# Kernel tuning notes

Hardware: AMD Instinct MI355X
Metric: run time of the kernel (lower is better)

Reference implementation:

```python
import jax, jax.numpy as jnp
import numpy as np
from jax import lax

B, C, H, W = 32, 64, 128, 128   # c must equal max_in_channels (see view in forward)
OUT, K = 64, 3
HIDDEN = 128


def setup_inputs() -> dict:
    key = jax.random.key(0)
    k1, k2, k3, k4, k5 = jax.random.split(key, 5)
    x = jax.random.normal(k1, (B, C, H, W), dtype=jnp.float32)
    # torch Linear default init scale ~ 1/sqrt(fan_in); use small scale for stability
    W1 = jax.random.normal(k2, (C, HIDDEN), dtype=jnp.float32) * (1.0 / np.sqrt(C))
    b1 = jax.random.normal(k3, (HIDDEN,), dtype=jnp.float32) * 0.01
    W2 = jax.random.normal(k4, (HIDDEN, OUT * C * K * K), dtype=jnp.float32) * (1.0 / np.sqrt(HIDDEN))
    b2 = jax.random.normal(k5, (OUT * C * K * K,), dtype=jnp.float32) * 0.01
    return {"x": x, "W1": W1, "b1": b1, "W2": W2, "b2": b2}


def reference(x, W1, b1, W2, b2):
    b, c, h, w = x.shape
    # per-sample channel statistics -> weight-generator MLP
    stats = jnp.mean(x, axis=(2, 3))                       # [b, c]
    hidden = jax.nn.relu(stats @ W1 + b1)                  # [b, hidden]
    weight = (hidden @ W2 + b2).reshape(b, OUT, c, K, K)   # per-sample conv kernels
    # batched per-sample conv expressed as one grouped convolution:
    # group i convolves sample i's channels with sample i's kernels
    lhs = x.reshape(1, b * c, h, w)                        # [1, b*c, H, W]
    rhs = weight.reshape(b * OUT, c, K, K)                 # [b*OUT, c, K, K]
    pad = K // 2
    out = lax.conv_general_dilated(
        lhs, rhs,
        window_strides=(1, 1),
        padding=[(pad, pad), (pad, pad)],
        feature_group_count=b,
        dimension_numbers=("NCHW", "OIHW", "NCHW"),
    )
    return out.reshape(b, OUT, h, w)
```

## Files before the change

### kernel.cpp

```cpp
#include <hip/hip_runtime.h>

typedef unsigned short u16;
typedef unsigned int   u32;
typedef __attribute__((ext_vector_type(8))) short short8v;
typedef __attribute__((ext_vector_type(4))) float float4v;
typedef __attribute__((address_space(1))) u32 g_u32;
typedef __attribute__((address_space(3))) u32 l_u32;


__device__ __forceinline__ u16 f2bf(float f) {
  u32 u = __builtin_bit_cast(u32, f);
  return (u16)((u + 0x7fffu + ((u >> 16) & 1u)) >> 16);
}

__global__ void __launch_bounds__(256) k_transpose_stats(
    const float* __restrict__ x, float* __restrict__ statsum, u16* __restrict__ xt)
{
  __shared__ u16 tile[64 * 130];
  const int b = blockIdx.x >> 7, y = blockIdx.x & 127;
  const int tid = threadIdx.x;
  const int c = tid >> 2, part = tid & 3, xb = part * 32;
  const float* src = x + (((size_t)(b * 64 + c) * 128 + y) * 128 + xb);
  float sum = 0.f;
  #pragma unroll
  for (int i = 0; i < 32; i += 4) {
    float4 v = *(const float4*)(src + i);
    sum += (v.x + v.y) + (v.z + v.w);
    ushort2 p01; p01.x = f2bf(v.x); p01.y = f2bf(v.y);
    ushort2 p23; p23.x = f2bf(v.z); p23.y = f2bf(v.w);
    *(ushort2*)&tile[c * 130 + xb + i]     = p01;
    *(ushort2*)&tile[c * 130 + xb + i + 2] = p23;
  }
  sum += __shfl_xor(sum, 1);
  sum += __shfl_xor(sum, 2);
  if (part == 0) atomicAdd(&statsum[b * 64 + c], sum);
  __syncthreads();

  uint4* xtv = (uint4*)xt;
  const size_t rowg = ((size_t)b * 130 + (y + 1)) * 1024;
  #pragma unroll
  for (int d0 = 0; d0 < 1024; d0 += 256) {
    const int d = d0 + tid;
    const int xd = d >> 3, s = d & 7;
    const int c8 = s ^ (xd & 7);
    const u16* tp = &tile[c8 * 8 * 130 + xd];
    u16 v0 = tp[0 * 130], v1 = tp[1 * 130], v2 = tp[2 * 130], v3 = tp[3 * 130];
    u16 v4 = tp[4 * 130], v5 = tp[5 * 130], v6 = tp[6 * 130], v7 = tp[7 * 130];
    uint4 g;
    g.x = (u32)v0 | ((u32)v1 << 16);
    g.y = (u32)v2 | ((u32)v3 << 16);
    g.z = (u32)v4 | ((u32)v5 << 16);
    g.w = (u32)v6 | ((u32)v7 << 16);
    xtv[rowg + d] = g;
  }
  if (y == 0 || y == 127) {
    const size_t prow = ((size_t)b * 130 + (y == 0 ? 0 : 129)) * 1024;
    uint4 z; z.x = z.y = z.z = z.w = 0u;
    #pragma unroll
    for (int d0 = 0; d0 < 1024; d0 += 256) xtv[prow + d0 + tid] = z;
  }
}

__global__ void __launch_bounds__(128) k_hidden(
    const float* __restrict__ statsum, const float* __restrict__ W1,
    const float* __restrict__ b1, float* __restrict__ hidden)
{
  const int b = blockIdx.x, h = threadIdx.x;
  float s = b1[h];
  #pragma unroll 4
  for (int c = 0; c < 64; ++c)
    s = fmaf(statsum[b * 64 + c] * (1.f / 16384.f), W1[c * 128 + h], s);
  hidden[b * 128 + h] = fmaxf(s, 0.f);
}

__global__ void __launch_bounds__(256) k_weightgen(
    const float* __restrict__ hidden, const float* __restrict__ W2,
    const float* __restrict__ b2, u16* __restrict__ wt)
{
  const int idx = blockIdx.x * 256 + threadIdx.x;
  const int b = idx >> 12, o = (idx >> 6) & 63, c = idx & 63;
  const int j0 = (o * 64 + c) * 9;
  float acc[9];
  #pragma unroll
  for (int t = 0; t < 9; ++t) acc[t] = b2[j0 + t];
  const float* hb = hidden + b * 128;
  for (int h = 0; h < 128; ++h) {
    const float hv = hb[h];
    const float* w2p = W2 + (size_t)h * 36864 + j0;
    #pragma unroll
    for (int t = 0; t < 9; ++t) acc[t] = fmaf(hv, w2p[t], acc[t]);
  }
  const int cc = c >> 5, cr = c & 31;
  #pragma unroll
  for (int kidx = 0; kidx < 9; ++kidx) {
    const size_t widx = ((size_t)(((b * 9 + kidx) * 2 + cc) * 64 + o)) * 32 + cr;
    wt[widx] = f2bf(acc[kidx]);
  }
}

__global__ void __launch_bounds__(256) k_conv(
    const u16* __restrict__ xt, const u16* __restrict__ wt, float* __restrict__ out)
{
  __shared__ u16 xs[4 * 1024 * 8];
  const int blk = blockIdx.x;
  const int b = blk >> 6, r = blk & 63;
  const int y0 = r * 2;
  const int tid = threadIdx.x;

  {
    const size_t srcg = ((size_t)b * 130 + y0) * 1024;
    #pragma unroll
    for (int k2 = 0; k2 < 16; ++k2) {
      const int g = k2 * 256 + tid;
      const void* gsrc = (const char*)xt + (srcg + (size_t)g) * 16;
      void* ldst = (char*)xs + (size_t)g * 16;
#if defined(__has_builtin) && __has_builtin(__builtin_amdgcn_global_load_lds)
      __builtin_amdgcn_global_load_lds((const g_u32*)gsrc, (l_u32*)ldst, 16, 0, 0);
#else
      *(uint4*)ldst = *(const uint4*)gsrc;
#endif
    }
  }
  __syncthreads();

  const int lane = tid & 63, wid = tid >> 6;
  const int lo = lane & 15, q = lane >> 4;
  const int yout = y0 + (wid >> 1);
  const int colbase = (wid & 1) * 64;

  const short8v z8 = {0, 0, 0, 0, 0, 0, 0, 0};
  float4v acc[4][4];
  {
    const float4v z4 = {0.f, 0.f, 0.f, 0.f};
    #pragma unroll
    for (int mt = 0; mt < 4; ++mt)
      #pragma unroll
      for (int nt = 0; nt < 4; ++nt) acc[mt][nt] = z4;
  }

  const size_t wbase = (size_t)b * 36864 + (size_t)(lo * 32 + q * 8);
  short8v a_cur[4];
  {
    const u16* p = wt + wbase;
    #pragma unroll
    for (int mt = 0; mt < 4; ++mt) a_cur[mt] = *(const short8v*)(p + mt * 512);
  }

  #pragma unroll 1
  for (int chunk = 0; chunk < 18; ++chunk) {
    const int kidx = chunk >> 1, cc = chunk & 1;
    const int ky = kidx / 3, kx = kidx - ky * 3;

    short8v a_nxt[4];
    if (chunk < 17) {
      const u16* p = wt + wbase + (size_t)(chunk + 1) * 2048;
      #pragma unroll
      for (int mt = 0; mt < 4; ++mt) a_nxt[mt] = *(const short8v*)(p + mt * 512);
    }

    const int row_l = (wid >> 1) + ky;
    const int c8 = cc * 4 + q;
    short8v bv[4];
    #pragma unroll
    for (int nt = 0; nt < 4; ++nt) {
      const int xin = colbase + nt * 16 + lo + kx - 1;
      const bool okx = ((unsigned)xin < 128u);
      const int gpos = okx ? (row_l * 1024 + xin * 8 + (c8 ^ (xin & 7))) : 0;
      short8v v = *(const short8v*)(xs + (size_t)gpos * 8);
      bv[nt] = okx ? v : z8;
    }

    #pragma unroll
    for (int mt = 0; mt < 4; ++mt)
      #pragma unroll
      for (int nt = 0; nt < 4; ++nt)
        acc[mt][nt] = __builtin_amdgcn_mfma_f32_16x16x32_bf16(
            a_cur[mt], bv[nt], acc[mt][nt], 0, 0, 0);

    if (chunk < 17) {
      #pragma unroll
      for (int mt = 0; mt < 4; ++mt) a_cur[mt] = a_nxt[mt];
    }
  }

  #pragma unroll
  for (int mt = 0; mt < 4; ++mt) {
    #pragma unroll
    for (int i = 0; i < 4; ++i) {
      const int o = mt * 16 + q * 4 + i;
      float* orow = out + ((size_t)(b * 64 + o) * 128 + yout) * 128;
      #pragma unroll
      for (int nt = 0; nt < 4; ++nt)
        orow[colbase + nt * 16 + lo] = acc[mt][nt][i];
    }
  }
}

extern "C" void kernel_launch(void* const* d_in, const int* in_sizes, int n_in,
                              void* d_out, int out_size, void* d_ws, size_t ws_size,
                              hipStream_t stream) {
  (void)in_sizes; (void)n_in; (void)out_size; (void)ws_size;
  const float* x  = (const float*)d_in[0];
  const float* W1 = (const float*)d_in[1];
  const float* b1 = (const float*)d_in[2];
  const float* W2 = (const float*)d_in[3];
  const float* b2 = (const float*)d_in[4];
  float* out = (float*)d_out;

  float* statsum = (float*)d_ws;
  float* hidden  = (float*)((char*)d_ws + 8192);
  u16*   wt      = (u16*)((char*)d_ws + 32768);
  u16*   xt      = (u16*)((char*)d_ws + (size_t)(4 << 20));

  hipMemsetAsync(statsum, 0, 2048 * sizeof(float), stream);
  k_transpose_stats<<<32 * 128, 256, 0, stream>>>(x, statsum, xt);
  k_hidden<<<32, 128, 0, stream>>>(statsum, W1, b1, hidden);
  k_weightgen<<<512, 256, 0, stream>>>(hidden, W2, b2, wt);
  k_conv<<<32 * 64, 256, 0, stream>>>(xt, wt, out);
}
```

Baseline: 353.6 us.

## Restructure weight generator so each W2 element is loaded once for all batches

The weight-generation GEMM is reorganised so each thread owns one output column j of W2 and accumulates all 32 batch samples, with the hidden dimension split across four wavefronts and reduced through shared memory. The hidden activations are stored transposed so every wave reads a contiguous row of 32 batch values, and the grid is resized to cover all 36864 columns. Before, each thread read 9 strided W2 values per hidden unit and W2 was re-read once per batch sample. Now W2, about 18 MB, is streamed once with coalesced loads. The cost is 32 accumulators per thread plus a shared-memory reduction and one barrier.

```diff
diff --git a/kernel.cpp b/kernel.cpp
--- a/kernel.cpp
+++ b/kernel.cpp
@@ -63,38 +63,57 @@
 
 __global__ void __launch_bounds__(128) k_hidden(
     const float* __restrict__ statsum, const float* __restrict__ W1,
-    const float* __restrict__ b1, float* __restrict__ hidden)
+    const float* __restrict__ b1, float* __restrict__ hiddenT)
 {
   const int b = blockIdx.x, h = threadIdx.x;
   float s = b1[h];
   #pragma unroll 4
   for (int c = 0; c < 64; ++c)
     s = fmaf(statsum[b * 64 + c] * (1.f / 16384.f), W1[c * 128 + h], s);
-  hidden[b * 128 + h] = fmaxf(s, 0.f);
+  hiddenT[h * 32 + b] = fmaxf(s, 0.f);
 }
 
 __global__ void __launch_bounds__(256) k_weightgen(
-    const float* __restrict__ hidden, const float* __restrict__ W2,
+    const float* __restrict__ hiddenT, const float* __restrict__ W2,
     const float* __restrict__ b2, u16* __restrict__ wt)
 {
-  const int idx = blockIdx.x * 256 + threadIdx.x;
-  const int b = idx >> 12, o = (idx >> 6) & 63, c = idx & 63;
-  const int j0 = (o * 64 + c) * 9;
-  float acc[9];
-  #pragma unroll
-  for (int t = 0; t < 9; ++t) acc[t] = b2[j0 + t];
-  const float* hb = hidden + b * 128;
-  for (int h = 0; h < 128; ++h) {
-    const float hv = hb[h];
-    const float* w2p = W2 + (size_t)h * 36864 + j0;
-    #pragma unroll
-    for (int t = 0; t < 9; ++t) acc[t] = fmaf(hv, w2p[t], acc[t]);
-  }
-  const int cc = c >> 5, cr = c & 31;
-  #pragma unroll
-  for (int kidx = 0; kidx < 9; ++kidx) {
-    const size_t widx = ((size_t)(((b * 9 + kidx) * 2 + cc) * 64 + o)) * 32 + cr;
-    wt[widx] = f2bf(acc[kidx]);
+  __shared__ float red[4][64][32];
+  const int tid = threadIdx.x;
+  const int hg = __builtin_amdgcn_readfirstlane(tid >> 6);
+  const int jl = tid & 63;
+  const int j = blockIdx.x * 64 + jl;
+
+  float acc[32];
+  #pragma unroll
+  for (int b = 0; b < 32; ++b) acc[b] = 0.f;
+
+  const float* __restrict__ hbase = hiddenT + hg * 32 * 32;
+  const float* __restrict__ wcol  = W2 + (size_t)hg * 32 * 36864 + j;
+  #pragma unroll 2
+  for (int hh = 0; hh < 32; ++hh) {
+    const float w = wcol[(size_t)hh * 36864];
+    const float* hr = hbase + hh * 32;
+    #pragma unroll
+    for (int b = 0; b < 32; ++b) acc[b] = fmaf(w, hr[b], acc[b]);
+  }
+
+  #pragma unroll
+  for (int b = 0; b < 32; ++b) red[hg][jl][(b + jl) & 31] = acc[b];
+  __syncthreads();
+
+  const int jr = tid & 63, b0 = (tid >> 6) * 8;
+  const int jj = blockIdx.x * 64 + jr;
+  const int oc = jj / 9, kidx = jj - oc * 9;
+  const int o = oc >> 6, c = oc & 63, cc2 = c >> 5, cr = c & 31;
+  const float bias = b2[jj];
+  #pragma unroll
+  for (int i = 0; i < 8; ++i) {
+    const int b = b0 + i;
+    const int rot = (b + jr) & 31;
+    float s = bias + red[0][jr][rot] + red[1][jr][rot]
+                   + red[2][jr][rot] + red[3][jr][rot];
+    const size_t widx = ((size_t)(((b * 9 + kidx) * 2 + cc2) * 64 + o)) * 32 + cr;
+    wt[widx] = f2bf(s);
   }
 }
 
@@ -208,13 +227,13 @@
   float* out = (float*)d_out;
 
   float* statsum = (float*)d_ws;
-  float* hidden  = (float*)((char*)d_ws + 8192);
+  float* hiddenT = (float*)((char*)d_ws + 8192);
   u16*   wt      = (u16*)((char*)d_ws + 32768);
   u16*   xt      = (u16*)((char*)d_ws + (size_t)(4 << 20));
 
   hipMemsetAsync(statsum, 0, 2048 * sizeof(float), stream);
   k_transpose_stats<<<32 * 128, 256, 0, stream>>>(x, statsum, xt);
-  k_hidden<<<32, 128, 0, stream>>>(statsum, W1, b1, hidden);
-  k_weightgen<<<512, 256, 0, stream>>>(hidden, W2, b2, wt);
+  k_hidden<<<32, 128, 0, stream>>>(statsum, W1, b1, hiddenT);
+  k_weightgen<<<576, 256, 0, stream>>>(hiddenT, W2, b2, wt);
   k_conv<<<32 * 64, 256, 0, stream>>>(xt, wt, out);
 }
```

New measurement: 335.1 us. 1.05x faster.
